# Kernel optimization log

Hardware: AMD Instinct MI355X
Metric: run time of the kernel (lower is better)

The kernel has to match this reference:

```python
import jax, jax.numpy as jnp
import numpy as np

B, S, H, NH = 4, 2048, 1024, 16
D = H // NH

def setup_inputs() -> dict:
    key = jax.random.key(0)
    ks = jax.random.split(key, 9)
    sc = 1.0 / np.sqrt(H)
    return {
        "x": jax.random.normal(ks[0], (B, S, H), jnp.float32),
        "Wq": jax.random.normal(ks[1], (H, H), jnp.float32) * sc,
        "bq": jax.random.normal(ks[2], (H,), jnp.float32) * 0.01,
        "Wk": jax.random.normal(ks[3], (H, H), jnp.float32) * sc,
        "bk": jax.random.normal(ks[4], (H,), jnp.float32) * 0.01,
        "Wv": jax.random.normal(ks[5], (H, H), jnp.float32) * sc,
        "bv": jax.random.normal(ks[6], (H,), jnp.float32) * 0.01,
        "Wo": jax.random.normal(ks[7], (H, H), jnp.float32) * sc,
        "bo": jax.random.normal(ks[8], (H,), jnp.float32) * 0.01,
    }

def reference(x, Wq, bq, Wk, bk, Wv, bv, Wo, bo):
    # torch Linear: y = x @ W.T + b
    def proj(x, W, b):
        # [B,S,H] -> [B,NH,S,D]
        y = jnp.einsum('bsh,oh->bso', x, W) + b
        return y.reshape(B, S, NH, D).transpose(0, 2, 1, 3)
    q = proj(x, Wq, bq)
    k = proj(x, Wk, bk)
    v = proj(x, Wv, bv)
    scores = jnp.einsum('bhqd,bhkd->bhqk', q, k) / jnp.sqrt(jnp.float32(D))
    p = jax.nn.softmax(scores, axis=-1)  # [B,NH,S,S]
    o = jnp.einsum('bhqk,bhkd->bhqd', p, v)  # dropout p=0 (eval)
    o = o.transpose(0, 2, 1, 3).reshape(B, S, H)
    return jnp.einsum('bsh,oh->bso', o, Wo) + bo
```

## Files before the change

kernel.cpp:

```cpp
#include <hip/hip_runtime.h>


#define DEV __device__ __forceinline__

typedef __bf16 bf16x8 __attribute__((ext_vector_type(8)));
typedef __bf16 bf16x4 __attribute__((ext_vector_type(4)));
typedef float floatx4 __attribute__((ext_vector_type(4)));

constexpr int Bdim = 4, SS = 2048, HH = 1024, NHH = 16, DD = 64;
constexpr int MM = Bdim * SS;

DEV void async16(const void* g, void* l) {
  __builtin_amdgcn_global_load_lds(
      (const __attribute__((address_space(1))) unsigned int*)g,
      (__attribute__((address_space(3))) unsigned int*)l, 16, 0, 0);
}

DEV int swz2(int r) { return (r ^ (r >> 2)) & 3; }
DEV int swz3(int r) { return (r ^ (r >> 3)) & 7; }

__global__ __launch_bounds__(256) void cast_bf16_kernel(
    const float* __restrict__ x, const float* __restrict__ wq,
    const float* __restrict__ wk, const float* __restrict__ wv,
    const float* __restrict__ wo,
    __bf16* __restrict__ xb, __bf16* __restrict__ wqb, __bf16* __restrict__ wkb,
    __bf16* __restrict__ wvb, __bf16* __restrict__ wob) {
  const float* src; __bf16* dst; int n4;
  switch (blockIdx.z) {
    case 0: src = x;  dst = xb;  n4 = MM * HH / 4; break;
    case 1: src = wq; dst = wqb; n4 = HH * HH / 4; break;
    case 2: src = wk; dst = wkb; n4 = HH * HH / 4; break;
    case 3: src = wv; dst = wvb; n4 = HH * HH / 4; break;
    default: src = wo; dst = wob; n4 = HH * HH / 4; break;
  }
  int stride = gridDim.x * blockDim.x;
  for (int i = blockIdx.x * blockDim.x + threadIdx.x; i < n4; i += stride) {
    float4 v = ((const float4*)src)[i];
    bf16x4 o;
    o[0] = (__bf16)v.x; o[1] = (__bf16)v.y; o[2] = (__bf16)v.z; o[3] = (__bf16)v.w;
    ((bf16x4*)dst)[i] = o;
  }
}

DEV void gemm_db128(const __bf16* __restrict__ Ablk, const __bf16* __restrict__ Bblk,
                    __bf16* As, __bf16* Bs, floatx4 acc[4][4]) {
  const int t = threadIdx.x;
  const int lane = t & 63, quad = lane >> 4, l16 = lane & 15;
  const int wid = t >> 6;
  const int wm = (wid >> 1) * 64, wn = (wid & 1) * 64;

  const int srow = t >> 2, sc = t & 3;
  const __bf16* Ag0 = Ablk + (size_t)srow * HH + (sc ^ swz2(srow)) * 8;
  const __bf16* Ag1 = Ablk + (size_t)(srow + 64) * HH + (sc ^ swz2(srow + 64)) * 8;
  const __bf16* Bg0 = Bblk + (size_t)srow * HH + (sc ^ swz2(srow)) * 8;
  const __bf16* Bg1 = Bblk + (size_t)(srow + 64) * HH + (sc ^ swz2(srow + 64)) * 8;

  int aoff[4], boff[4];
#pragma unroll
  for (int i = 0; i < 4; ++i) {
    int ra = wm + i * 16 + l16;
    aoff[i] = ra * 32 + (quad ^ swz2(ra)) * 8;
    int rb = wn + i * 16 + l16;
    boff[i] = rb * 32 + (quad ^ swz2(rb)) * 8;
  }

  async16(Ag0, As + t * 8);
  async16(Ag1, As + 2048 + t * 8);
  async16(Bg0, Bs + t * 8);
  async16(Bg1, Bs + 2048 + t * 8);

  for (int it = 0; it < HH / 32; ++it) {
    const int cur = it & 1;
    __syncthreads();

    if (it + 1 < HH / 32) {
      const int k = (it + 1) * 32;
      const int nxt = (cur ^ 1) * 4096;
      async16(Ag0 + k, As + nxt + t * 8);
      async16(Ag1 + k, As + nxt + 2048 + t * 8);
      async16(Bg0 + k, Bs + nxt + t * 8);
      async16(Bg1 + k, Bs + nxt + 2048 + t * 8);
    }

    bf16x8 af[4], bfr[4];
#pragma unroll
    for (int i = 0; i < 4; ++i) {
      af[i]  = *(const bf16x8*)&As[cur * 4096 + aoff[i]];
      bfr[i] = *(const bf16x8*)&Bs[cur * 4096 + boff[i]];
    }
#pragma unroll
    for (int mi = 0; mi < 4; ++mi)
#pragma unroll
      for (int ni = 0; ni < 4; ++ni)
        acc[mi][ni] = __builtin_amdgcn_mfma_f32_16x16x32_bf16(af[mi], bfr[ni],
                                                              acc[mi][ni], 0, 0, 0);
  }
}

DEV void gemm128(const __bf16* __restrict__ Ablk, const __bf16* __restrict__ Bblk,
                 __bf16* As, __bf16* Bs, floatx4 acc[4][4]) {
  const int t = threadIdx.x;
  const int lane = t & 63, quad = lane >> 4, l16 = lane & 15;
  const int wid = t >> 6;
  const int wm = (wid >> 1) * 64, wn = (wid & 1) * 64;

  const int srow = t >> 2, sc = t & 3;
  const __bf16* Ag0 = Ablk + (size_t)srow * HH + (sc ^ swz2(srow)) * 8;
  const __bf16* Ag1 = Ablk + (size_t)(srow + 64) * HH + (sc ^ swz2(srow + 64)) * 8;
  const __bf16* Bg0 = Bblk + (size_t)srow * HH + (sc ^ swz2(srow)) * 8;
  const __bf16* Bg1 = Bblk + (size_t)(srow + 64) * HH + (sc ^ swz2(srow + 64)) * 8;
  __bf16* AsW = As + t * 8;
  __bf16* BsW = Bs + t * 8;

  int aoff[4], boff[4];
#pragma unroll
  for (int i = 0; i < 4; ++i) {
    int ra = wm + i * 16 + l16;
    aoff[i] = ra * 32 + (quad ^ swz2(ra)) * 8;
    int rb = wn + i * 16 + l16;
    boff[i] = rb * 32 + (quad ^ swz2(rb)) * 8;
  }

  for (int k0 = 0; k0 < HH; k0 += 32) {
    async16(Ag0 + k0, AsW);
    async16(Ag1 + k0, AsW + 2048);
    async16(Bg0 + k0, BsW);
    async16(Bg1 + k0, BsW + 2048);
    __syncthreads();
    bf16x8 af[4], bfr[4];
#pragma unroll
    for (int i = 0; i < 4; ++i) {
      af[i]  = *(const bf16x8*)&As[aoff[i]];
      bfr[i] = *(const bf16x8*)&Bs[boff[i]];
    }
#pragma unroll
    for (int mi = 0; mi < 4; ++mi)
#pragma unroll
      for (int ni = 0; ni < 4; ++ni)
        acc[mi][ni] = __builtin_amdgcn_mfma_f32_16x16x32_bf16(af[mi], bfr[ni],
                                                              acc[mi][ni], 0, 0, 0);
    __syncthreads();
  }
}

__global__ __launch_bounds__(256) void proj_qkv_kernel(
    const __bf16* __restrict__ xb,
    const __bf16* __restrict__ wqb, const __bf16* __restrict__ wkb,
    const __bf16* __restrict__ wvb,
    const float* __restrict__ bq, const float* __restrict__ bk,
    const float* __restrict__ bv,
    __bf16* __restrict__ Q, __bf16* __restrict__ Kc, __bf16* __restrict__ Vt) {
  __shared__ __align__(16) __bf16 As[2 * 128 * 32];
  __shared__ __align__(16) __bf16 Bs[2 * 128 * 32];
  const int mode = blockIdx.z;
  const __bf16* W = mode == 0 ? wqb : mode == 1 ? wkb : wvb;
  const float* bias = mode == 0 ? bq : mode == 1 ? bk : bv;
  const int m0 = blockIdx.y * 128, n0 = blockIdx.x * 128;

  floatx4 acc[4][4] = {};
  gemm_db128(xb + (size_t)m0 * HH, W + (size_t)n0 * HH, As, Bs, acc);

  const int t = threadIdx.x, lane = t & 63, quad = lane >> 4, l16 = lane & 15;
  const int wid = t >> 6, wm = (wid >> 1) * 64, wn = (wid & 1) * 64;
  const float qscale = 0.125f * 1.44269504088896f;
#pragma unroll
  for (int ni = 0; ni < 4; ++ni) {
    int n = n0 + wn + ni * 16 + l16;
    float bval = bias[n];
    int h = n >> 6, d = n & 63;
#pragma unroll
    for (int mi = 0; mi < 4; ++mi) {
      int mbase = m0 + wm + mi * 16 + quad * 4;
      int bb = mbase >> 11, sbase = mbase & (SS - 1);
      size_t bh = (size_t)(bb * NHH + h);
      if (mode == 2) {
        bf16x4 pv;
#pragma unroll
        for (int r = 0; r < 4; ++r) pv[r] = (__bf16)(acc[mi][ni][r] + bval);
        *(bf16x4*)&Vt[(bh * DD + d) * SS + sbase] = pv;
      } else {
#pragma unroll
        for (int r = 0; r < 4; ++r) {
          float v = acc[mi][ni][r] + bval;
          if (mode == 0) Q [(bh * SS + sbase + r) * DD + d] = (__bf16)(v * qscale);
          else           Kc[(bh * SS + sbase + r) * DD + d] = (__bf16)v;
        }
      }
    }
  }
}

__global__ __launch_bounds__(256) void proj_out_kernel(
    const __bf16* __restrict__ Ob, const __bf16* __restrict__ wob,
    const float* __restrict__ bo, float* __restrict__ out) {
  __shared__ __align__(16) __bf16 As[128 * 32];
  __shared__ __align__(16) __bf16 Bs[128 * 32];
  const int m0 = blockIdx.y * 128, n0 = blockIdx.x * 128;
  floatx4 acc[4][4] = {};
  gemm128(Ob + (size_t)m0 * HH, wob + (size_t)n0 * HH, As, Bs, acc);
  const int t = threadIdx.x, lane = t & 63, quad = lane >> 4, l16 = lane & 15;
  const int wid = t >> 6, wm = (wid >> 1) * 64, wn = (wid & 1) * 64;
#pragma unroll
  for (int ni = 0; ni < 4; ++ni) {
    int n = n0 + wn + ni * 16 + l16;
    float bval = bo[n];
#pragma unroll
    for (int mi = 0; mi < 4; ++mi)
#pragma unroll
      for (int r = 0; r < 4; ++r) {
        int m = m0 + wm + mi * 16 + quad * 4 + r;
        out[(size_t)m * HH + n] = acc[mi][ni][r] + bval;
      }
  }
}

__global__ __launch_bounds__(256, 2) void attn_kernel(
    const __bf16* __restrict__ Q, const __bf16* __restrict__ Kc,
    const __bf16* __restrict__ Vt, __bf16* __restrict__ Ob) {
  __shared__ __align__(16) __bf16 Ks[2][64 * 64];
  __shared__ __align__(16) __bf16 Vs[2][64 * 64];
  __shared__ __align__(16) __bf16 Ps[4 * 64 * 40];

  const int t = threadIdx.x, lane = t & 63, quad = lane >> 4, l16 = lane & 15;
  const int wid = t >> 6;
  const int qt = blockIdx.x, h = blockIdx.y, b = blockIdx.z;
  const size_t bh = (size_t)b * NHH + h;
  const __bf16* Qg = Q + (bh * SS + (size_t)qt * 256) * DD;
  const __bf16* Kg = Kc + bh * SS * DD;
  const __bf16* Vg = Vt + bh * DD * SS;

  const int srow = t >> 3;
  const int sc = t & 7;

  const __bf16* KgA = Kg + (size_t)srow * DD + (sc ^ swz3(srow)) * 8;
  const __bf16* KgB = Kg + (size_t)(srow + 32) * DD + (sc ^ swz3(srow + 32)) * 8;
  const __bf16* VgA = Vg + (size_t)srow * SS + (sc ^ swz3(srow)) * 8;
  const __bf16* VgB = Vg + (size_t)(srow + 32) * SS + (sc ^ swz3(srow + 32)) * 8;

  bf16x8 qf[4][2];
#pragma unroll
  for (int ni = 0; ni < 4; ++ni)
#pragma unroll
    for (int ks = 0; ks < 2; ++ks)
      qf[ni][ks] = *(const bf16x8*)(Qg + (size_t)(wid * 64 + ni * 16 + l16) * DD
                                    + (ks * 4 + quad) * 8);

  floatx4 oacc[4][4] = {};
  float rsum[4] = {0.f, 0.f, 0.f, 0.f};

  __bf16* Pw = Ps + wid * (64 * 40);

  int koff[4][2];
#pragma unroll
  for (int mi = 0; mi < 4; ++mi) {
    int r = mi * 16 + l16;
#pragma unroll
    for (int ks = 0; ks < 2; ++ks)
      koff[mi][ks] = r * 64 + ((ks * 4 + quad) ^ swz3(r)) * 8;
  }

  async16(KgA, &Ks[0][t * 8]);
  async16(KgB, &Ks[0][2048 + t * 8]);
  async16(VgA, &Vs[0][t * 8]);
  async16(VgB, &Vs[0][2048 + t * 8]);

  for (int kt = 0; kt < SS / 64; ++kt) {
    const int cur = kt & 1;
    __syncthreads();

    if (kt + 1 < SS / 64) {
      const int kk = (kt + 1) * 64;
      const int nxt = cur ^ 1;
      async16(KgA + (size_t)kk * DD, &Ks[nxt][t * 8]);
      async16(KgB + (size_t)kk * DD, &Ks[nxt][2048 + t * 8]);
      async16(VgA + kk, &Vs[nxt][t * 8]);
      async16(VgB + kk, &Vs[nxt][2048 + t * 8]);
    }

    floatx4 sacc[4][4];
#pragma unroll
    for (int mi = 0; mi < 4; ++mi)
#pragma unroll
      for (int ni = 0; ni < 4; ++ni) sacc[mi][ni] = floatx4{0.f, 0.f, 0.f, 0.f};
#pragma unroll
    for (int ks = 0; ks < 2; ++ks) {
      bf16x8 kf[4];
#pragma unroll
      for (int mi = 0; mi < 4; ++mi) kf[mi] = *(const bf16x8*)&Ks[cur][koff[mi][ks]];
#pragma unroll
      for (int mi = 0; mi < 4; ++mi)
#pragma unroll
        for (int ni = 0; ni < 4; ++ni)
          sacc[mi][ni] = __builtin_amdgcn_mfma_f32_16x16x32_bf16(kf[mi], qf[ni][ks],
                                                                 sacc[mi][ni], 0, 0, 0);
    }

#pragma unroll
    for (int hf = 0; hf < 2; ++hf) {
#pragma unroll
      for (int mh = 0; mh < 2; ++mh) {
        const int mi = hf * 2 + mh;
#pragma unroll
        for (int ni = 0; ni < 4; ++ni) {
          bf16x4 pk;
#pragma unroll
          for (int r = 0; r < 4; ++r) {
            float p = __builtin_amdgcn_exp2f(sacc[mi][ni][r]);
            rsum[ni] += p;
            pk[r] = (__bf16)p;
          }
          *(bf16x4*)&Pw[(ni * 16 + l16) * 40 + mh * 16 + quad * 4] = pk;
        }
      }
      bf16x8 ap[4], bv8[4];
#pragma unroll
      for (int mq = 0; mq < 4; ++mq)
        ap[mq] = *(const bf16x8*)&Pw[(mq * 16 + l16) * 40 + quad * 8];
#pragma unroll
      for (int nj = 0; nj < 4; ++nj) bv8[nj] = *(const bf16x8*)&Vs[cur][koff[nj][hf]];
#pragma unroll
      for (int mq = 0; mq < 4; ++mq)
#pragma unroll
        for (int nj = 0; nj < 4; ++nj)
          oacc[mq][nj] = __builtin_amdgcn_mfma_f32_16x16x32_bf16(ap[mq], bv8[nj],
                                                                 oacc[mq][nj], 0, 0, 0);
    }
  }

#pragma unroll
  for (int ni = 0; ni < 4; ++ni) {
    rsum[ni] += __shfl_xor(rsum[ni], 16, 64);
    rsum[ni] += __shfl_xor(rsum[ni], 32, 64);
  }

  const int s0 = qt * 256 + wid * 64;
#pragma unroll
  for (int mq = 0; mq < 4; ++mq) {
#pragma unroll
    for (int r = 0; r < 4; ++r) {
      float inv = 1.f / __shfl(rsum[mq], quad * 4 + r, 64);
      int s = s0 + mq * 16 + quad * 4 + r;
#pragma unroll
      for (int nj = 0; nj < 4; ++nj) {
        int d = nj * 16 + l16;
        Ob[((size_t)b * SS + s) * HH + h * DD + d] = (__bf16)(oacc[mq][nj][r] * inv);
      }
    }
  }
}

extern "C" void kernel_launch(void* const* d_in, const int* in_sizes, int n_in,
                              void* d_out, int out_size, void* d_ws, size_t ws_size,
                              hipStream_t stream) {
  const float* x  = (const float*)d_in[0];
  const float* Wq = (const float*)d_in[1];
  const float* bq = (const float*)d_in[2];
  const float* Wk = (const float*)d_in[3];
  const float* bk = (const float*)d_in[4];
  const float* Wv = (const float*)d_in[5];
  const float* bv = (const float*)d_in[6];
  const float* Wo = (const float*)d_in[7];
  const float* bo = (const float*)d_in[8];
  float* out = (float*)d_out;

  char* ws = (char*)d_ws;
  __bf16* xb  = (__bf16*)(ws);
  __bf16* wqb = (__bf16*)(ws + 16777216);
  __bf16* wkb = (__bf16*)(ws + 18874368);
  __bf16* wvb = (__bf16*)(ws + 20971520);
  __bf16* wob = (__bf16*)(ws + 23068672);
  __bf16* Qb  = (__bf16*)(ws + 25165824);
  __bf16* Kb  = (__bf16*)(ws + 41943040);
  __bf16* Vtb = (__bf16*)(ws + 58720256);
  __bf16* Ob  = (__bf16*)(ws + 75497472);

  cast_bf16_kernel<<<dim3(256, 1, 5), 256, 0, stream>>>(x, Wq, Wk, Wv, Wo,
                                                        xb, wqb, wkb, wvb, wob);
  proj_qkv_kernel<<<dim3(8, 64, 3), 256, 0, stream>>>(xb, wqb, wkb, wvb,
                                                      bq, bk, bv, Qb, Kb, Vtb);
  attn_kernel<<<dim3(8, 16, 4), 256, 0, stream>>>(Qb, Kb, Vtb, Ob);
  proj_out_kernel<<<dim3(8, 64), 256, 0, stream>>>(Ob, wob, bo, out);
}
```

Before: 297.1 us.

## Fuse QKV projections into one block sharing the X tile with XCD-aware mapping

The QKV projection kernel now computes Q, K and V for one 128x64 output tile in a single block, so each loaded X tile is reused across all three weight matrices instead of being reloaded three times. The launch becomes a flat 1024-block grid, with an index mapping that groups M tiles per XCD to improve L2 locality, and launch bounds request 3 blocks per CU. The trade-offs are more accumulator registers (24 fragments) and a smaller N tile per weight.

```diff
diff --git a/kernel.cpp b/kernel.cpp
--- a/kernel.cpp
+++ b/kernel.cpp
@@ -42,32 +42,54 @@
   }
 }
 
-DEV void gemm_db128(const __bf16* __restrict__ Ablk, const __bf16* __restrict__ Bblk,
-                    __bf16* As, __bf16* Bs, floatx4 acc[4][4]) {
+__global__ __launch_bounds__(256, 3) void proj_qkv_kernel(
+    const __bf16* __restrict__ xb,
+    const __bf16* __restrict__ wqb, const __bf16* __restrict__ wkb,
+    const __bf16* __restrict__ wvb,
+    const float* __restrict__ bq, const float* __restrict__ bk,
+    const float* __restrict__ bv,
+    __bf16* __restrict__ Q, __bf16* __restrict__ Kc, __bf16* __restrict__ Vt) {
+  __shared__ __align__(16) __bf16 As[2][128 * 32];
+  __shared__ __align__(16) __bf16 Bs[2][3][64 * 32];
+
+  const int lid = blockIdx.x;
+  const int xcd = lid & 7, slot = lid >> 3;
+  const int mp = xcd + 8 * (slot >> 4);
+  const int np = slot & 15;
+  const int m0 = mp * 128, n0 = np * 64;
+
   const int t = threadIdx.x;
   const int lane = t & 63, quad = lane >> 4, l16 = lane & 15;
   const int wid = t >> 6;
-  const int wm = (wid >> 1) * 64, wn = (wid & 1) * 64;
+
+  const __bf16* const Wm[3] = {wqb, wkb, wvb};
 
   const int srow = t >> 2, sc = t & 3;
-  const __bf16* Ag0 = Ablk + (size_t)srow * HH + (sc ^ swz2(srow)) * 8;
-  const __bf16* Ag1 = Ablk + (size_t)(srow + 64) * HH + (sc ^ swz2(srow + 64)) * 8;
-  const __bf16* Bg0 = Bblk + (size_t)srow * HH + (sc ^ swz2(srow)) * 8;
-  const __bf16* Bg1 = Bblk + (size_t)(srow + 64) * HH + (sc ^ swz2(srow + 64)) * 8;
-
-  int aoff[4], boff[4];
-#pragma unroll
-  for (int i = 0; i < 4; ++i) {
-    int ra = wm + i * 16 + l16;
-    aoff[i] = ra * 32 + (quad ^ swz2(ra)) * 8;
-    int rb = wn + i * 16 + l16;
-    boff[i] = rb * 32 + (quad ^ swz2(rb)) * 8;
-  }
-
-  async16(Ag0, As + t * 8);
-  async16(Ag1, As + 2048 + t * 8);
-  async16(Bg0, Bs + t * 8);
-  async16(Bg1, Bs + 2048 + t * 8);
+  const __bf16* Ag0 = xb + (size_t)(m0 + srow) * HH + (sc ^ swz2(srow)) * 8;
+  const __bf16* Ag1 = xb + (size_t)(m0 + srow + 64) * HH + (sc ^ swz2(srow + 64)) * 8;
+  const __bf16* Bg[3];
+#pragma unroll
+  for (int mo = 0; mo < 3; ++mo)
+    Bg[mo] = Wm[mo] + (size_t)(n0 + srow) * HH + (sc ^ swz2(srow)) * 8;
+
+  int aoff[2], boff[4];
+#pragma unroll
+  for (int mi = 0; mi < 2; ++mi) {
+    int ra = wid * 32 + mi * 16 + l16;
+    aoff[mi] = ra * 32 + (quad ^ swz2(ra)) * 8;
+  }
+#pragma unroll
+  for (int ni = 0; ni < 4; ++ni) {
+    int rb = ni * 16 + l16;
+    boff[ni] = rb * 32 + (quad ^ swz2(rb)) * 8;
+  }
+
+  floatx4 acc[3][2][4] = {};
+
+  async16(Ag0, &As[0][t * 8]);
+  async16(Ag1, &As[0][2048 + t * 8]);
+#pragma unroll
+  for (int mo = 0; mo < 3; ++mo) async16(Bg[mo], &Bs[0][mo][t * 8]);
 
   for (int it = 0; it < HH / 32; ++it) {
     const int cur = it & 1;
@@ -75,25 +97,59 @@
 
     if (it + 1 < HH / 32) {
       const int k = (it + 1) * 32;
-      const int nxt = (cur ^ 1) * 4096;
-      async16(Ag0 + k, As + nxt + t * 8);
-      async16(Ag1 + k, As + nxt + 2048 + t * 8);
-      async16(Bg0 + k, Bs + nxt + t * 8);
-      async16(Bg1 + k, Bs + nxt + 2048 + t * 8);
-    }
-
-    bf16x8 af[4], bfr[4];
-#pragma unroll
-    for (int i = 0; i < 4; ++i) {
-      af[i]  = *(const bf16x8*)&As[cur * 4096 + aoff[i]];
-      bfr[i] = *(const bf16x8*)&Bs[cur * 4096 + boff[i]];
-    }
-#pragma unroll
-    for (int mi = 0; mi < 4; ++mi)
-#pragma unroll
-      for (int ni = 0; ni < 4; ++ni)
-        acc[mi][ni] = __builtin_amdgcn_mfma_f32_16x16x32_bf16(af[mi], bfr[ni],
-                                                              acc[mi][ni], 0, 0, 0);
+      const int nxt = cur ^ 1;
+      async16(Ag0 + k, &As[nxt][t * 8]);
+      async16(Ag1 + k, &As[nxt][2048 + t * 8]);
+#pragma unroll
+      for (int mo = 0; mo < 3; ++mo) async16(Bg[mo] + k, &Bs[nxt][mo][t * 8]);
+    }
+
+    bf16x8 af[2];
+#pragma unroll
+    for (int mi = 0; mi < 2; ++mi) af[mi] = *(const bf16x8*)&As[cur][aoff[mi]];
+#pragma unroll
+    for (int mo = 0; mo < 3; ++mo) {
+      bf16x8 bfr[4];
+#pragma unroll
+      for (int ni = 0; ni < 4; ++ni) bfr[ni] = *(const bf16x8*)&Bs[cur][mo][boff[ni]];
+#pragma unroll
+      for (int mi = 0; mi < 2; ++mi)
+#pragma unroll
+        for (int ni = 0; ni < 4; ++ni)
+          acc[mo][mi][ni] = __builtin_amdgcn_mfma_f32_16x16x32_bf16(
+              af[mi], bfr[ni], acc[mo][mi][ni], 0, 0, 0);
+    }
+  }
+
+  const float qscale = 0.125f * 1.44269504088896f;
+#pragma unroll
+  for (int mo = 0; mo < 3; ++mo) {
+    const float* bias = mo == 0 ? bq : mo == 1 ? bk : bv;
+#pragma unroll
+    for (int ni = 0; ni < 4; ++ni) {
+      int n = n0 + ni * 16 + l16;
+      float bval = bias[n];
+      int h = n >> 6, d = n & 63;
+#pragma unroll
+      for (int mi = 0; mi < 2; ++mi) {
+        int mbase = m0 + wid * 32 + mi * 16 + quad * 4;
+        int bb = mbase >> 11, sbase = mbase & (SS - 1);
+        size_t bh = (size_t)(bb * NHH + h);
+        if (mo == 2) {
+          bf16x4 pv;
+#pragma unroll
+          for (int r = 0; r < 4; ++r) pv[r] = (__bf16)(acc[mo][mi][ni][r] + bval);
+          *(bf16x4*)&Vt[(bh * DD + d) * SS + sbase] = pv;
+        } else {
+#pragma unroll
+          for (int r = 0; r < 4; ++r) {
+            float v = acc[mo][mi][ni][r] + bval;
+            if (mo == 0) Q [(bh * SS + sbase + r) * DD + d] = (__bf16)(v * qscale);
+            else         Kc[(bh * SS + sbase + r) * DD + d] = (__bf16)v;
+          }
+        }
+      }
+    }
   }
 }
 
@@ -140,53 +196,6 @@
         acc[mi][ni] = __builtin_amdgcn_mfma_f32_16x16x32_bf16(af[mi], bfr[ni],
                                                               acc[mi][ni], 0, 0, 0);
     __syncthreads();
-  }
-}
-
-__global__ __launch_bounds__(256) void proj_qkv_kernel(
-    const __bf16* __restrict__ xb,
-    const __bf16* __restrict__ wqb, const __bf16* __restrict__ wkb,
-    const __bf16* __restrict__ wvb,
-    const float* __restrict__ bq, const float* __restrict__ bk,
-    const float* __restrict__ bv,
-    __bf16* __restrict__ Q, __bf16* __restrict__ Kc, __bf16* __restrict__ Vt) {
-  __shared__ __align__(16) __bf16 As[2 * 128 * 32];
-  __shared__ __align__(16) __bf16 Bs[2 * 128 * 32];
-  const int mode = blockIdx.z;
-  const __bf16* W = mode == 0 ? wqb : mode == 1 ? wkb : wvb;
-  const float* bias = mode == 0 ? bq : mode == 1 ? bk : bv;
-  const int m0 = blockIdx.y * 128, n0 = blockIdx.x * 128;
-
-  floatx4 acc[4][4] = {};
-  gemm_db128(xb + (size_t)m0 * HH, W + (size_t)n0 * HH, As, Bs, acc);
-
-  const int t = threadIdx.x, lane = t & 63, quad = lane >> 4, l16 = lane & 15;
-  const int wid = t >> 6, wm = (wid >> 1) * 64, wn = (wid & 1) * 64;
-  const float qscale = 0.125f * 1.44269504088896f;
-#pragma unroll
-  for (int ni = 0; ni < 4; ++ni) {
-    int n = n0 + wn + ni * 16 + l16;
-    float bval = bias[n];
-    int h = n >> 6, d = n & 63;
-#pragma unroll
-    for (int mi = 0; mi < 4; ++mi) {
-      int mbase = m0 + wm + mi * 16 + quad * 4;
-      int bb = mbase >> 11, sbase = mbase & (SS - 1);
-      size_t bh = (size_t)(bb * NHH + h);
-      if (mode == 2) {
-        bf16x4 pv;
-#pragma unroll
-        for (int r = 0; r < 4; ++r) pv[r] = (__bf16)(acc[mi][ni][r] + bval);
-        *(bf16x4*)&Vt[(bh * DD + d) * SS + sbase] = pv;
-      } else {
-#pragma unroll
-        for (int r = 0; r < 4; ++r) {
-          float v = acc[mi][ni][r] + bval;
-          if (mode == 0) Q [(bh * SS + sbase + r) * DD + d] = (__bf16)(v * qscale);
-          else           Kc[(bh * SS + sbase + r) * DD + d] = (__bf16)v;
-        }
-      }
-    }
   }
 }
 
@@ -376,8 +385,8 @@
 
   cast_bf16_kernel<<<dim3(256, 1, 5), 256, 0, stream>>>(x, Wq, Wk, Wv, Wo,
                                                         xb, wqb, wkb, wvb, wob);
-  proj_qkv_kernel<<<dim3(8, 64, 3), 256, 0, stream>>>(xb, wqb, wkb, wvb,
-                                                      bq, bk, bv, Qb, Kb, Vtb);
+  proj_qkv_kernel<<<dim3(1024), 256, 0, stream>>>(xb, wqb, wkb, wvb,
+                                                  bq, bk, bv, Qb, Kb, Vtb);
   attn_kernel<<<dim3(8, 16, 4), 256, 0, stream>>>(Qb, Kb, Vtb, Ob);
   proj_out_kernel<<<dim3(8, 64), 256, 0, stream>>>(Ob, wob, bo, out);
 }
```

After: 287.2 us. 3.3% less time.
